# Kernel optimization log

Measured on AMD Instinct MI355X. Metric: run time of the kernel, lower is better.

Reference implementation:

```python
import jax, jax.numpy as jnp
import numpy as np

THRESHOLD = 0.5
SLACK = 3
EPS = 1e-12
B, H, W = 16, 512, 512


def _shift(p, dy, dx, b, h, w):
    # p is zero-padded by 1 on spatial dims; returns neighbor at offset (dy, dx)
    return p[:, 1 + dy:1 + dy + h, 1 + dx:1 + dx + w]


def _thin_sub(img, step):
    # One Zhang-Suen sub-iteration on bool image [B,H,W] (zero boundary, as skimage)
    b, h, w = img.shape
    p = jnp.pad(img.astype(jnp.int32), ((0, 0), (1, 1), (1, 1)))
    # P2..P9 clockwise starting at North
    P2 = _shift(p, -1, 0, b, h, w); P3 = _shift(p, -1, 1, b, h, w)
    P4 = _shift(p, 0, 1, b, h, w);  P5 = _shift(p, 1, 1, b, h, w)
    P6 = _shift(p, 1, 0, b, h, w);  P7 = _shift(p, 1, -1, b, h, w)
    P8 = _shift(p, 0, -1, b, h, w); P9 = _shift(p, -1, -1, b, h, w)
    seq = [P2, P3, P4, P5, P6, P7, P8, P9, P2]
    Bn = P2 + P3 + P4 + P5 + P6 + P7 + P8 + P9          # neighbor count
    A = sum((1 - seq[k]) * seq[k + 1] for k in range(8))  # 0->1 transitions
    cond = (Bn >= 2) & (Bn <= 6) & (A == 1)
    if step == 0:
        cond = cond & (P2 * P4 * P6 == 0) & (P4 * P6 * P8 == 0)
    else:
        cond = cond & (P2 * P4 * P8 == 0) & (P2 * P6 * P8 == 0)
    return img & ~cond


def _skeletonize(img):
    # Iterate Zhang-Suen thinning to convergence (skimage.morphology.skeletonize 2D = Zhang's method)
    def body(state):
        cur, _ = state
        nxt = _thin_sub(_thin_sub(cur, 0), 1)
        return (nxt, jnp.any(nxt != cur))

    out, _ = jax.lax.while_loop(lambda s: s[1], body, (img, jnp.array(True)))
    return out


def _edt_sq(mask):
    # Exact squared Euclidean distance to nearest True pixel, separable 2-pass.
    b, h, w = mask.shape
    BIG = h + w  # larger than any attainable 1D distance
    g = jnp.where(mask, 0, BIG).astype(jnp.int32)  # [B,H,W]

    # pass 1: 1D nearest-True distance along rows (axis=1) via fwd/bwd scans
    def fscan(carry, row):
        d = jnp.minimum(row, carry + 1)
        return d, d

    g_rows = jnp.moveaxis(g, 1, 0)  # [H,B,W]
    init = jnp.full((b, w), BIG, jnp.int32)
    _, fwd = jax.lax.scan(fscan, init, g_rows)
    _, bwd = jax.lax.scan(fscan, init, g_rows[::-1])
    f = jnp.minimum(jnp.minimum(fwd, bwd[::-1]), BIG)  # [H,B,W]
    f2 = jnp.moveaxis(f * f, 0, 1)  # [B,H,W] squared vertical distance

    # pass 2: d2[b,i,j] = min_{j'} f2[b,i,j'] + (j-j')^2 (lower envelope, memory-friendly lax.map)
    js = jnp.arange(w, dtype=jnp.int32)

    def one_col(j):
        off = (js - j) ** 2  # [W]
        return jnp.min(f2 + off[None, None, :], axis=-1)  # [B,H]

    d2 = jax.lax.map(one_col, js)  # [W,B,H]
    return jnp.transpose(d2, (1, 2, 0))  # [B,H,W]


def setup_inputs() -> dict:
    key = jax.random.key(0)
    k1, k2 = jax.random.split(key)
    y_pred = jax.random.uniform(k1, (B, H, W), dtype=jnp.float32)
    y_true = jax.random.uniform(k2, (B, H, W), dtype=jnp.float32)
    return {"y_pred": y_pred, "y_true": y_true}


def reference(y_pred, y_true):
    p = y_pred > THRESHOLD  # greater_is_road=True binarization
    g = y_true > THRESHOLD
    p = _skeletonize(p)
    g = _skeletonize(g)
    d2_gt = _edt_sq(g)   # EDT of ~g == distance to nearest g pixel
    d2_pr = _edt_sq(p)
    s2 = SLACK * SLACK   # dist <= slack  <=>  dist^2 <= slack^2 (integer sq EDT)
    tp_area = d2_gt <= s2
    fp_area = ~tp_area
    fn_area = d2_pr > s2
    ax = (1, 2)
    TP = jnp.sum(tp_area & p, ax).astype(jnp.float32)
    FP = jnp.sum(fp_area & p, ax).astype(jnp.float32)
    FN = jnp.sum(fn_area & g, ax).astype(jnp.float32)
    correctness = TP / (TP + FP + EPS)
    completeness = TP / (TP + FN + EPS)
    quality = TP / (TP + FP + FN + EPS)
    # mean over batch -> [3]: [correctness, completeness, quality]
    return jnp.mean(jnp.stack([correctness, completeness, quality], axis=1), axis=0)
```

## Files before the change

### kernel.cpp

```cpp
#include <hip/hip_runtime.h>
#include <stdint.h>

#define HH 512
#define WW 512
#define HW (HH * WW)
#define WPR 8
#define NWORDS (HH * WPR)
#define NTHREADS 1024
#define NB 16

#define LSTR 10
#define LROWS (HH + 2)
#define LWORDS (LROWS * LSTR)

typedef unsigned long long u64;

__device__ __forceinline__ u64 zs_core(u64 cc, u64 P2, u64 P3, u64 P4, u64 P5,
                                       u64 P6, u64 P7, u64 P8, u64 P9, int step) {
    u64 ab = P2 ^ P3;
    u64 s1 = ab ^ P4, c1 = (P2 & P3) | (ab & P4);
    u64 de = P5 ^ P6;
    u64 s2 = de ^ P7, c2 = (P5 & P6) | (de & P7);
    u64 s3 = P8 ^ P9, c3 = P8 & P9;
    u64 gh = s1 ^ s2;
    u64 b0 = gh ^ s3, c4 = (s1 & s2) | (gh & s3);
    u64 ij = c1 ^ c2;
    u64 s4 = ij ^ c3, c5 = (c1 & c2) | (ij & c3);
    u64 b1 = s4 ^ c4, c6 = s4 & c4;
    u64 b2 = c5 ^ c6, b3 = c5 & c6;

    u64 Bge2 = b1 | b2 | b3;
    u64 Ble6 = ~(b3 | (b2 & b1 & b0));

    u64 a1, a2, t;
    t = ~P2 & P3; a1 = t; a2 = 0ULL;
    t = ~P3 & P4; a2 |= a1 & t; a1 |= t;
    t = ~P4 & P5; a2 |= a1 & t; a1 |= t;
    t = ~P5 & P6; a2 |= a1 & t; a1 |= t;
    t = ~P6 & P7; a2 |= a1 & t; a1 |= t;
    t = ~P7 & P8; a2 |= a1 & t; a1 |= t;
    t = ~P8 & P9; a2 |= a1 & t; a1 |= t;
    t = ~P9 & P2; a2 |= a1 & t; a1 |= t;
    u64 Aeq1 = a1 & ~a2;

    u64 sccond = (step == 0) ? ~((P4 & P6) & (P2 | P8))
                             : ~((P2 & P8) & (P4 | P6));

    return cc & ~(Bge2 & Ble6 & Aeq1 & sccond);
}

__global__ __launch_bounds__(256)
void pack_kernel(const float* __restrict__ y_pred,
                 const float* __restrict__ y_true,
                 u64* __restrict__ bits ,
                 int* __restrict__ cnt ) {
    int tid = threadIdx.x;
    if (blockIdx.x == 0 && tid < 4 * NB) cnt[tid] = 0;

    int t = blockIdx.x * 256 + tid;
    size_t g0 = (size_t)t * 16;
    const float* src;
    size_t off;
    if (g0 < (size_t)NB * HW) { src = y_pred; off = g0; }
    else                      { src = y_true; off = g0 - (size_t)NB * HW; }
    const float4* s4 = (const float4*)(src + off);
    float4 a = s4[0];
    float4 b = s4[1];
    float4 c = s4[2];
    float4 d = s4[3];
    unsigned m =
        ((unsigned)(a.x > 0.5f) << 0)  | ((unsigned)(a.y > 0.5f) << 1)  |
        ((unsigned)(a.z > 0.5f) << 2)  | ((unsigned)(a.w > 0.5f) << 3)  |
        ((unsigned)(b.x > 0.5f) << 4)  | ((unsigned)(b.y > 0.5f) << 5)  |
        ((unsigned)(b.z > 0.5f) << 6)  | ((unsigned)(b.w > 0.5f) << 7)  |
        ((unsigned)(c.x > 0.5f) << 8)  | ((unsigned)(c.y > 0.5f) << 9)  |
        ((unsigned)(c.z > 0.5f) << 10) | ((unsigned)(c.w > 0.5f) << 11) |
        ((unsigned)(d.x > 0.5f) << 12) | ((unsigned)(d.y > 0.5f) << 13) |
        ((unsigned)(d.z > 0.5f) << 14) | ((unsigned)(d.w > 0.5f) << 15);
    ((unsigned short*)bits)[t] = (unsigned short)m;
}

__global__ __launch_bounds__(NTHREADS, 4)
void skel_kernel(u64* __restrict__ bits ) {
    __shared__ u64 Mb[2][LWORDS];
    __shared__ unsigned int Cpb[2][130];
    __shared__ int s_any[3];

    int bx = blockIdx.x;
    int tid = threadIdx.x;
    int lane = tid & 63;
    int c = tid & 7;
    int rb = tid >> 3;

    u64* gm = bits + (size_t)bx * NWORDS;

    if (tid < LROWS) {
        int i = tid;
        if (i == 0 || i == LROWS - 1) {
            #pragma unroll
            for (int j = 0; j < LSTR; ++j) { Mb[0][i * LSTR + j] = 0; Mb[1][i * LSTR + j] = 0; }
        } else {
            Mb[0][i * LSTR + 0] = 0; Mb[0][i * LSTR + 9] = 0;
            Mb[1][i * LSTR + 0] = 0; Mb[1][i * LSTR + 9] = 0;
        }
    }

    {
        const ulonglong2* s2 = (const ulonglong2*)gm;
        #pragma unroll
        for (int k = 0; k < 2; ++k) {
            int i = k * NTHREADS + tid;
            ulonglong2 v = s2[i];
            int wi = i * 2;
            int r = wi >> 3, c2 = wi & 7;
            int li = (r + 1) * LSTR + c2 + 1;
            Mb[0][li] = v.x;
            Mb[0][li + 1] = v.y;
        }
    }

    if (tid < 130) {
        Cpb[0][tid] = (tid >= 1 && tid <= 128) ? 0x1FEu : 0u;
        Cpb[1][tid] = 0u;
    }
    if (tid < 3) s_any[tid] = 0;

    unsigned dl = 0x1FEu;
    bool prevchg = true;
    int base = (rb * 4 + 1) * LSTR + (c + 1);

    int it = 0;
    bool done = false;
    for (;;) {
        for (int step = 0; step < 2; ++step) {
            __syncthreads();
            if (step == 0 && it > 0) {
                if (s_any[(it + 2) % 3] == 0) { done = true; break; }
            }
            const u64* Ms = Mb[step];
            u64* Md = Mb[step ^ 1];
            const unsigned* CpS = Cpb[step];
            unsigned* CpD = Cpb[step ^ 1];

            unsigned need = ((CpS[rb] | CpS[rb + 1] | CpS[rb + 2]) >> c) & 7u;
            bool chg = false;
            if (need) {
                u64 Ca, Ea, Wa, Cb, Eb, Wb, Cc, Ec, Wc;
                {   int a = base - LSTR;
                    u64 x = Ms[a], mm = Ms[a - 1], pp = Ms[a + 1];
                    Ca = x; Ea = (x >> 1) | (pp << 63); Wa = (x << 1) | (mm >> 63); }
                {   int a = base;
                    u64 x = Ms[a], mm = Ms[a - 1], pp = Ms[a + 1];
                    Cb = x; Eb = (x >> 1) | (pp << 63); Wb = (x << 1) | (mm >> 63); }
                u64 nv0 = 0, nv1 = 0, nv2 = 0, nv3 = 0;

                {   int a = base + LSTR;
                    u64 x = Ms[a], mm = Ms[a - 1], pp = Ms[a + 1];
                    Cc = x; Ec = (x >> 1) | (pp << 63); Wc = (x << 1) | (mm >> 63);
                    if (Cb) nv0 = zs_core(Cb, Ca, Ea, Eb, Ec, Cc, Wc, Wb, Wa, step);
                    chg |= (nv0 != Cb);
                    Ca = Cb; Ea = Eb; Wa = Wb; Cb = Cc; Eb = Ec; Wb = Wc; }
                {   int a = base + 2 * LSTR;
                    u64 x = Ms[a], mm = Ms[a - 1], pp = Ms[a + 1];
                    Cc = x; Ec = (x >> 1) | (pp << 63); Wc = (x << 1) | (mm >> 63);
                    if (Cb) nv1 = zs_core(Cb, Ca, Ea, Eb, Ec, Cc, Wc, Wb, Wa, step);
                    chg |= (nv1 != Cb);
                    Ca = Cb; Ea = Eb; Wa = Wb; Cb = Cc; Eb = Ec; Wb = Wc; }
                {   int a = base + 3 * LSTR;
                    u64 x = Ms[a], mm = Ms[a - 1], pp = Ms[a + 1];
                    Cc = x; Ec = (x >> 1) | (pp << 63); Wc = (x << 1) | (mm >> 63);
                    if (Cb) nv2 = zs_core(Cb, Ca, Ea, Eb, Ec, Cc, Wc, Wb, Wa, step);
                    chg |= (nv2 != Cb);
                    Ca = Cb; Ea = Eb; Wa = Wb; Cb = Cc; Eb = Ec; Wb = Wc; }
                {   int a = base + 4 * LSTR;
                    u64 x = Ms[a], mm = Ms[a - 1], pp = Ms[a + 1];
                    Cc = x; Ec = (x >> 1) | (pp << 63); Wc = (x << 1) | (mm >> 63);
                    if (Cb) nv3 = zs_core(Cb, Ca, Ea, Eb, Ec, Cc, Wc, Wb, Wa, step);
                    chg |= (nv3 != Cb); }

                if (chg | prevchg) {
                    Md[base] = nv0;
                    Md[base + LSTR] = nv1;
                    Md[base + 2 * LSTR] = nv2;
                    Md[base + 3 * LSTR] = nv3;
                }
            }
            prevchg = chg;

            u64 bal = __ballot(chg);
            if (bal && lane == 0) s_any[it % 3] = 1;
            if ((lane & 7) == 0) {
                unsigned byte = ((unsigned)(bal >> lane) & 0xFFu) << 1;
                CpD[rb + 1] = byte | dl;
                dl = byte;
            }
            if (step == 1 && tid == 0) s_any[(it + 1) % 3] = 0;
        }
        if (done || it >= 1024) break;
        ++it;
    }

    {
        ulonglong2* d2 = (ulonglong2*)gm;
        #pragma unroll
        for (int k = 0; k < 2; ++k) {
            int i = k * NTHREADS + tid;
            int wi = i * 2;
            int r = wi >> 3, c2 = wi & 7;
            int li = (r + 1) * LSTR + c2 + 1;
            ulonglong2 v;
            v.x = Mb[0][li];
            v.y = Mb[0][li + 1];
            d2[i] = v;
        }
    }
}

#define STRIPS 8
#define SROWS (HH / STRIPS)
#define SR2 (SROWS + 6)

__device__ __forceinline__ u64 ldws(const u64* M, int r, int c) {
    return (c < 0 || c >= WPR) ? 0ULL : M[r * WPR + c];
}

__device__ __forceinline__ u64 dil3s(const u64* M, int r, int c) {
    u64 cm = ldws(M, r, c - 1), cc = ldws(M, r, c), cp = ldws(M, r, c + 1);
    u64 h = cc
          | (cc >> 1) | (cp << 63)
          | (cc >> 2) | (cp << 62)
          | (cc >> 3) | (cp << 61)
          | (cc << 1) | (cm >> 63)
          | (cc << 2) | (cm >> 62)
          | (cc << 3) | (cm >> 61);
    u64 um = ldws(M, r - 1, c - 1) | ldws(M, r + 1, c - 1) | ldws(M, r - 2, c - 1) | ldws(M, r + 2, c - 1);
    u64 uc = ldws(M, r - 1, c    ) | ldws(M, r + 1, c    ) | ldws(M, r - 2, c    ) | ldws(M, r + 2, c    );
    u64 up = ldws(M, r - 1, c + 1) | ldws(M, r + 1, c + 1) | ldws(M, r - 2, c + 1) | ldws(M, r + 2, c + 1);
    h |= uc
       | (uc >> 1) | (up << 63)
       | (uc >> 2) | (up << 62)
       | (uc << 1) | (um >> 63)
       | (uc << 2) | (um >> 62);
    h |= ldws(M, r - 3, c) | ldws(M, r + 3, c);
    return h;
}

__global__ __launch_bounds__(256)
void count_kernel(const u64* __restrict__ skel, int* __restrict__ cnt) {
    __shared__ u64 P[SR2 * WPR];
    __shared__ u64 G[SR2 * WPR];
    __shared__ int acc[4];

    int b = blockIdx.x / STRIPS;
    int s = blockIdx.x % STRIPS;
    int tid = threadIdx.x;
    int r0 = s * SROWS - 3;

    const u64* sp = skel + (size_t)b * NWORDS;
    const u64* sg = skel + (size_t)(NB + b) * NWORDS;
    for (int i = tid; i < SR2 * WPR; i += 256) {
        int gr = r0 + (i >> 3);
        bool in = (gr >= 0 && gr < HH);
        int gi = gr * WPR + (i & 7);
        P[i] = in ? sp[gi] : 0ULL;
        G[i] = in ? sg[gi] : 0ULL;
    }
    if (tid < 4) acc[tid] = 0;
    __syncthreads();

    int cp = 0, cg = 0, tp = 0, fnh = 0;
    #pragma unroll
    for (int k = 0; k < 2; ++k) {
        int w = k * 256 + tid;
        int r = (w >> 3) + 3, c = w & 7;
        u64 pw = P[r * WPR + c], gw = G[r * WPR + c];
        cp  += __popcll(pw);
        cg  += __popcll(gw);
        tp  += __popcll(pw & dil3s(G, r, c));
        fnh += __popcll(gw & dil3s(P, r, c));
    }
    #pragma unroll
    for (int o = 32; o > 0; o >>= 1) {
        cp  += __shfl_down(cp, o);
        cg  += __shfl_down(cg, o);
        tp  += __shfl_down(tp, o);
        fnh += __shfl_down(fnh, o);
    }
    if ((tid & 63) == 0) {
        atomicAdd(&acc[0], cp);
        atomicAdd(&acc[1], cg);
        atomicAdd(&acc[2], tp);
        atomicAdd(&acc[3], fnh);
    }
    __syncthreads();
    if (tid < 4) atomicAdd(&cnt[b * 4 + tid], acc[tid]);
}

__global__ void ccq_reduce(const int* __restrict__ cnt, float* __restrict__ out) {
    int k = threadIdx.x;
    if (k < 3) {
        float s = 0.0f;
        for (int b = 0; b < NB; ++b) {
            float TP = (float)cnt[b * 4 + 2];
            float FP = (float)(cnt[b * 4 + 0] - cnt[b * 4 + 2]);
            float FN = (float)(cnt[b * 4 + 1] - cnt[b * 4 + 3]);
            float v = (k == 0) ? TP / (TP + FP + 1e-12f)
                    : (k == 1) ? TP / (TP + FN + 1e-12f)
                               : TP / (TP + FP + FN + 1e-12f);
            s += v;
        }
        out[k] = s * (1.0f / NB);
    }
}

extern "C" void kernel_launch(void* const* d_in, const int* in_sizes, int n_in,
                              void* d_out, int out_size, void* d_ws, size_t ws_size,
                              hipStream_t stream) {
    (void)in_sizes; (void)n_in; (void)out_size; (void)ws_size;
    const float* y_pred = (const float*)d_in[0];
    const float* y_true = (const float*)d_in[1];
    float* out = (float*)d_out;

    u64* bits = (u64*)d_ws;
    int* cnt = (int*)((char*)d_ws + (size_t)2 * NB * NWORDS * sizeof(u64));

    hipLaunchKernelGGL(pack_kernel, dim3(2 * NB * HW / 16 / 256), dim3(256), 0, stream,
                       y_pred, y_true, bits, cnt);
    hipLaunchKernelGGL(skel_kernel, dim3(2 * NB), dim3(NTHREADS), 0, stream, bits);
    hipLaunchKernelGGL(count_kernel, dim3(NB * STRIPS), dim3(256), 0, stream,
                       bits, cnt);
    hipLaunchKernelGGL(ccq_reduce, dim3(1), dim3(64), 0, stream, cnt, out);
}
```

Baseline: 115.9 us.

## Split skeletonization into halo strip blocks and fuse final reduction into count kernel

```diff
diff --git a/kernel.cpp b/kernel.cpp
--- a/kernel.cpp
+++ b/kernel.cpp
@@ -8,6 +8,7 @@
 #define NWORDS (HH * WPR)
 #define NTHREADS 1024
 #define NB 16
+#define NIMG (2 * NB)
 
 #define LSTR 10
 #define LROWS (HH + 2)
@@ -55,7 +56,7 @@
                  u64* __restrict__ bits ,
                  int* __restrict__ cnt ) {
     int tid = threadIdx.x;
-    if (blockIdx.x == 0 && tid < 4 * NB) cnt[tid] = 0;
+    if (blockIdx.x == 0 && tid < 4 * NB + NIMG + 1) cnt[tid] = 0;
 
     int t = blockIdx.x * 256 + tid;
     size_t g0 = (size_t)t * 16;
@@ -80,13 +81,95 @@
     ((unsigned short*)bits)[t] = (unsigned short)m;
 }
 
+#define SSTRIPS 8
+#define SIROWS (HH / SSTRIPS)
+#define SHALO 24
+#define SDROWS (SIROWS + 2 * SHALO)
+#define STHREADS (SDROWS * WPR)
+#define SITERS (SHALO / 2)
+#define SSTR 10
+#define SLWORDS ((SDROWS + 2) * SSTR)
+
+__global__ __launch_bounds__(STHREADS)
+void strip_kernel(const u64* __restrict__ src, u64* __restrict__ dst,
+                  int* __restrict__ flags, int rec) {
+    __shared__ u64 Mb[2][SLWORDS];
+    __shared__ int s_any[3];
+
+    int bx = blockIdx.x;
+    int img = bx >> 3;
+    int s = bx & 7;
+    int tid = threadIdx.x;
+    int lane = tid & 63;
+    int r = tid >> 3;
+    int c = tid & 7;
+    int gr = s * SIROWS - SHALO + r;
+
+    for (int i = tid; i < SLWORDS; i += STHREADS) { Mb[0][i] = 0; Mb[1][i] = 0; }
+    if (tid < 3) s_any[tid] = 0;
+    __syncthreads();
+
+    const u64* gsrc = src + (size_t)img * NWORDS;
+    u64 v = (gr >= 0 && gr < HH) ? gsrc[gr * WPR + c] : 0ULL;
+    int base = (r + 1) * SSTR + (c + 1);
+    Mb[0][base] = v;
+
+    bool prevchg = true;
+    int it = 0;
+    bool done = false;
+    for (;;) {
+        for (int step = 0; step < 2; ++step) {
+            __syncthreads();
+            if (step == 0 && it > 0) {
+                if (s_any[(it + 2) % 3] == 0) { done = true; break; }
+            }
+            const u64* Ms = Mb[step];
+            u64* Md = Mb[step ^ 1];
+            u64 cc = Ms[base];
+            u64 nv = cc;
+            bool chg = false;
+            if (cc) {
+                u64 nm = Ms[base - SSTR - 1], nc = Ms[base - SSTR], np = Ms[base - SSTR + 1];
+                u64 cm = Ms[base - 1],                              cp = Ms[base + 1];
+                u64 sm = Ms[base + SSTR - 1], sc = Ms[base + SSTR], sp = Ms[base + SSTR + 1];
+                u64 P2 = nc;
+                u64 P3 = (nc >> 1) | (np << 63);
+                u64 P4 = (cc >> 1) | (cp << 63);
+                u64 P5 = (sc >> 1) | (sp << 63);
+                u64 P6 = sc;
+                u64 P7 = (sc << 1) | (sm >> 63);
+                u64 P8 = (cc << 1) | (cm >> 63);
+                u64 P9 = (nc << 1) | (nm >> 63);
+                nv = zs_core(cc, P2, P3, P4, P5, P6, P7, P8, P9, step);
+                chg = (nv != cc);
+            }
+            if (chg | prevchg) Md[base] = nv;
+            prevchg = chg;
+            u64 bal = __ballot(chg);
+            if (bal && lane == 0) s_any[it % 3] = 1;
+            if (step == 1 && tid == 0) s_any[(it + 1) % 3] = 0;
+        }
+        if (done) break;
+        if (++it >= SITERS) break;
+    }
+    __syncthreads();
+    int lastAny = done ? 0 : s_any[(SITERS - 1) % 3];
+
+    if (r >= SHALO && r < SHALO + SIROWS) {
+        dst[(size_t)img * NWORDS + gr * WPR + c] = Mb[0][base];
+    }
+    if (rec && lastAny && tid == 0) flags[img] = 1;
+}
+
 __global__ __launch_bounds__(NTHREADS, 4)
-void skel_kernel(u64* __restrict__ bits ) {
+void skel_kernel(u64* __restrict__ bits, const int* __restrict__ flags) {
     __shared__ u64 Mb[2][LWORDS];
     __shared__ unsigned int Cpb[2][130];
     __shared__ int s_any[3];
 
     int bx = blockIdx.x;
+    if (flags[bx] == 0) return;
+
     int tid = threadIdx.x;
     int lane = tid & 63;
     int c = tid & 7;
@@ -104,7 +187,6 @@
             Mb[1][i * LSTR + 0] = 0; Mb[1][i * LSTR + 9] = 0;
         }
     }
-
     {
         const ulonglong2* s2 = (const ulonglong2*)gm;
         #pragma unroll
@@ -118,7 +200,6 @@
             Mb[0][li + 1] = v.y;
         }
     }
-
     if (tid < 130) {
         Cpb[0][tid] = (tid >= 1 && tid <= 128) ? 0x1FEu : 0u;
         Cpb[1][tid] = 0u;
@@ -153,7 +234,6 @@
                     u64 x = Ms[a], mm = Ms[a - 1], pp = Ms[a + 1];
                     Cb = x; Eb = (x >> 1) | (pp << 63); Wb = (x << 1) | (mm >> 63); }
                 u64 nv0 = 0, nv1 = 0, nv2 = 0, nv3 = 0;
-
                 {   int a = base + LSTR;
                     u64 x = Ms[a], mm = Ms[a - 1], pp = Ms[a + 1];
                     Cc = x; Ec = (x >> 1) | (pp << 63); Wc = (x << 1) | (mm >> 63);
@@ -177,7 +257,6 @@
                     Cc = x; Ec = (x >> 1) | (pp << 63); Wc = (x << 1) | (mm >> 63);
                     if (Cb) nv3 = zs_core(Cb, Ca, Ea, Eb, Ec, Cc, Wc, Wb, Wa, step);
                     chg |= (nv3 != Cb); }
-
                 if (chg | prevchg) {
                     Md[base] = nv0;
                     Md[base + LSTR] = nv1;
@@ -186,7 +265,6 @@
                 }
             }
             prevchg = chg;
-
             u64 bal = __ballot(chg);
             if (bal && lane == 0) s_any[it % 3] = 1;
             if ((lane & 7) == 0) {
@@ -246,10 +324,12 @@
 }
 
 __global__ __launch_bounds__(256)
-void count_kernel(const u64* __restrict__ skel, int* __restrict__ cnt) {
+void count_kernel(const u64* __restrict__ skel, int* __restrict__ cnt,
+                  int* __restrict__ done, float* __restrict__ out) {
     __shared__ u64 P[SR2 * WPR];
     __shared__ u64 G[SR2 * WPR];
     __shared__ int acc[4];
+    __shared__ int s_last;
 
     int b = blockIdx.x / STRIPS;
     int s = blockIdx.x % STRIPS;
@@ -294,22 +374,30 @@
     }
     __syncthreads();
     if (tid < 4) atomicAdd(&cnt[b * 4 + tid], acc[tid]);
-}
-
-__global__ void ccq_reduce(const int* __restrict__ cnt, float* __restrict__ out) {
-    int k = threadIdx.x;
-    if (k < 3) {
-        float s = 0.0f;
-        for (int b = 0; b < NB; ++b) {
-            float TP = (float)cnt[b * 4 + 2];
-            float FP = (float)(cnt[b * 4 + 0] - cnt[b * 4 + 2]);
-            float FN = (float)(cnt[b * 4 + 1] - cnt[b * 4 + 3]);
-            float v = (k == 0) ? TP / (TP + FP + 1e-12f)
-                    : (k == 1) ? TP / (TP + FN + 1e-12f)
-                               : TP / (TP + FP + FN + 1e-12f);
-            s += v;
-        }
-        out[k] = s * (1.0f / NB);
+    __syncthreads();
+    if (tid == 0) {
+        __threadfence();
+        s_last = (atomicAdd(done, 1) == NB * STRIPS - 1);
+    }
+    __syncthreads();
+    if (!s_last) return;
+    __threadfence();
+
+    if (tid < 3) {
+        float sacc = 0.0f;
+        for (int i = 0; i < NB; ++i) {
+            float c0 = (float)atomicAdd(&cnt[i * 4 + 0], 0);
+            float c1 = (float)atomicAdd(&cnt[i * 4 + 1], 0);
+            float TP = (float)atomicAdd(&cnt[i * 4 + 2], 0);
+            float c3 = (float)atomicAdd(&cnt[i * 4 + 3], 0);
+            float FP = c0 - TP;
+            float FN = c1 - c3;
+            float v = (tid == 0) ? TP / (TP + FP + 1e-12f)
+                    : (tid == 1) ? TP / (TP + FN + 1e-12f)
+                                 : TP / (TP + FP + FN + 1e-12f);
+            sacc += v;
+        }
+        out[tid] = sacc * (1.0f / NB);
     }
 }
 
@@ -321,13 +409,20 @@
     const float* y_true = (const float*)d_in[1];
     float* out = (float*)d_out;
 
-    u64* bits = (u64*)d_ws;
-    int* cnt = (int*)((char*)d_ws + (size_t)2 * NB * NWORDS * sizeof(u64));
+    u64* buf1 = (u64*)d_ws;
+    u64* buf2 = buf1 + (size_t)NIMG * NWORDS;
+    int* cnt = (int*)(buf2 + (size_t)NIMG * NWORDS);
+    int* flags = cnt + 4 * NB;
+    int* done = flags + NIMG;
 
     hipLaunchKernelGGL(pack_kernel, dim3(2 * NB * HW / 16 / 256), dim3(256), 0, stream,
-                       y_pred, y_true, bits, cnt);
-    hipLaunchKernelGGL(skel_kernel, dim3(2 * NB), dim3(NTHREADS), 0, stream, bits);
+                       y_pred, y_true, buf1, cnt);
+    hipLaunchKernelGGL(strip_kernel, dim3(NIMG * SSTRIPS), dim3(STHREADS), 0, stream,
+                       buf1, buf2, flags, 0);
+    hipLaunchKernelGGL(strip_kernel, dim3(NIMG * SSTRIPS), dim3(STHREADS), 0, stream,
+                       buf2, buf1, flags, 1);
+    hipLaunchKernelGGL(skel_kernel, dim3(NIMG), dim3(NTHREADS), 0, stream,
+                       buf1, flags);
     hipLaunchKernelGGL(count_kernel, dim3(NB * STRIPS), dim3(256), 0, stream,
-                       bits, cnt);
-    hipLaunchKernelGGL(ccq_reduce, dim3(1), dim3(64), 0, stream, cnt, out);
-}
+                       buf1, cnt, done, out);
+}
```

Measured after the change: 117.9 us. No clear change (+1.7%).
